# Optimization experiments

Hardware: AMD Instinct MI355X
Metric: run time of the kernel (lower is better)

The kernel has to match this reference:

```python
import jax, jax.numpy as jnp
import numpy as np

N_NODES = 50000
N_EDGES = 800000
IN_DIM = 128
E_FEATS = 64
H = 8
D = IN_DIM // H
NEG_SLOPE = 0.2


def setup_inputs() -> dict:
    key = jax.random.key(0)
    ks = jax.random.split(key, 9)
    h = jax.random.normal(ks[0], (N_NODES, IN_DIM), dtype=jnp.float32)
    edge_features = jax.random.normal(ks[1], (N_EDGES, E_FEATS), dtype=jnp.float32)
    src = jax.random.randint(ks[2], (N_EDGES,), 0, N_NODES, dtype=jnp.int32)
    dst = jax.random.randint(ks[3], (N_EDGES,), 0, N_NODES, dtype=jnp.int32)
    s = 0.05
    Wq = jax.random.normal(ks[4], (IN_DIM, IN_DIM), dtype=jnp.float32) * s
    Wk = jax.random.normal(ks[5], (IN_DIM, IN_DIM), dtype=jnp.float32) * s
    Wv = jax.random.normal(ks[6], (IN_DIM, IN_DIM), dtype=jnp.float32) * s
    We = jax.random.normal(ks[7], (H, E_FEATS), dtype=jnp.float32) * s
    Wres = jax.random.normal(ks[8], (IN_DIM, IN_DIM), dtype=jnp.float32) * s
    return {"h": h, "edge_features": edge_features, "src": src, "dst": dst,
            "Wq": Wq, "Wk": Wk, "Wv": Wv, "We": We, "Wres": Wres}


def reference(h, edge_features, src, dst, Wq, Wk, Wv, We, Wres):
    N = h.shape[0]
    # QKV projections (feat_drop is identity at eval)
    q = (h @ Wq.T).reshape(N, H, D)
    k = (h @ Wk.T).reshape(N, H, D)
    v = (h @ Wv.T).reshape(N, H, D)
    # ee / m_att are computed in the original forward but never used (dead code)
    _ee = edge_features @ We.T  # [E, H]

    # v_dot_u('q','k'): dot(q[dst], k[src]) per edge, per head -> [E, H]
    e = jnp.einsum('ehd,ehd->eh', q[dst], k[src])
    e = jnp.where(e >= 0, e, NEG_SLOPE * e)  # leaky_relu

    # edge_softmax over incoming edges of each destination node
    m = jax.ops.segment_max(e, dst, num_segments=N)          # [N, H]
    ex = jnp.exp(e - m[dst])                                 # [E, H]
    z = jax.ops.segment_sum(ex, dst, num_segments=N)         # [N, H]
    alpha = ex / z[dst]                                      # [E, H] (attn_drop identity)

    # weighted aggregation: sum_e alpha * v[src]
    msg = v[src] * alpha[:, :, None]                         # [E, H, D]
    rst = jax.ops.segment_sum(msg, dst, num_segments=N)      # [N, H, D]
    rst = rst.reshape(N, H * D)
    rst = rst + h @ Wres.T                                   # residual
    return rst
```

## Files before the change

kernel.cpp:

```cpp
#include <hip/hip_runtime.h>


#define NEG_SLOPE 0.2f
#define CB 1024

typedef __attribute__((ext_vector_type(8))) short short8;
typedef __attribute__((ext_vector_type(4))) float f32x4;

__device__ __forceinline__ unsigned short f2bf(float f) {
    unsigned int u = __builtin_bit_cast(unsigned int, f);
    u = (u + 0x7fffu + ((u >> 16) & 1u)) >> 16;
    return (unsigned short)u;
}
__device__ __forceinline__ float bf2f(unsigned short s) {
    unsigned int u = (unsigned int)s << 16;
    return __builtin_bit_cast(float, u);
}

__global__ __launch_bounds__(256) void zero_wconv_kernel(
    const float* __restrict__ Wq, const float* __restrict__ Wk,
    const float* __restrict__ Wv, const float* __restrict__ Wres,
    unsigned short* __restrict__ wpk, int* __restrict__ cnt,
    int* __restrict__ csr_pad, int n4)
{
    int t = blockIdx.x * 256 + threadIdx.x;
    if (t < 8192) {
        int l = t & 63;
        int v = t >> 6;
        int kk = v & 3;
        int wct = v >> 2;
        int ct = wct & 7;
        int w = wct >> 3;
        const float* W = (w == 0) ? Wq : (w == 1) ? Wk : (w == 2) ? Wv : Wres;
        const float* srcp = W + (size_t)(ct * 16 + (l & 15)) * 128 + kk * 32 + (l >> 4) * 8;
        float4 lo = *reinterpret_cast<const float4*>(srcp);
        float4 hi = *reinterpret_cast<const float4*>(srcp + 4);
        short8 o;
        o[0] = (short)f2bf(lo.x); o[1] = (short)f2bf(lo.y);
        o[2] = (short)f2bf(lo.z); o[3] = (short)f2bf(lo.w);
        o[4] = (short)f2bf(hi.x); o[5] = (short)f2bf(hi.y);
        o[6] = (short)f2bf(hi.z); o[7] = (short)f2bf(hi.w);
        *reinterpret_cast<short8*>(wpk + (size_t)t * 8) = o;
        if (t < 64) csr_pad[t] = 0;
    } else {
        int u = t - 8192;
        if (u < n4) reinterpret_cast<int4*>(cnt)[u] = make_int4(0, 0, 0, 0);
    }
}

__global__ __launch_bounds__(256) void proj_count_kernel(
    const float* __restrict__ h,
    const unsigned short* __restrict__ wpk,
    unsigned short* __restrict__ qb, unsigned short* __restrict__ kb,
    signed char* __restrict__ vi8, float* __restrict__ vscl,
    unsigned short* __restrict__ resb,
    const int* __restrict__ dst, int* __restrict__ cnt,
    int N, int E, int PB)
{
    if (blockIdx.x >= PB) {
        int start = (blockIdx.x - PB) * 256 + threadIdx.x;
        for (int e = start; e < E; e += CB * 256)
            atomicAdd(&cnt[dst[e]], 1);
        return;
    }

    const int wid = threadIdx.x >> 6;
    const int lane = threadIdx.x & 63;
    const int row0 = blockIdx.x * 128 + wid * 32;
    const int r = lane & 15, g = lane >> 4;

    short8 afrag[2][4];
    #pragma unroll
    for (int grp = 0; grp < 2; ++grp) {
        int arow = row0 + grp * 16 + r;
        if (arow >= N) arow = N - 1;
        const float* hrow = h + (size_t)arow * 128 + g * 8;
        #pragma unroll
        for (int kk = 0; kk < 4; ++kk) {
            float4 lo = *reinterpret_cast<const float4*>(hrow + kk * 32);
            float4 hi = *reinterpret_cast<const float4*>(hrow + kk * 32 + 4);
            short8 a;
            a[0] = (short)f2bf(lo.x); a[1] = (short)f2bf(lo.y);
            a[2] = (short)f2bf(lo.z); a[3] = (short)f2bf(lo.w);
            a[4] = (short)f2bf(hi.x); a[5] = (short)f2bf(hi.y);
            a[6] = (short)f2bf(hi.z); a[7] = (short)f2bf(hi.w);
            afrag[grp][kk] = a;
        }
    }

    #pragma unroll
    for (int sec = 0; sec < 3; ++sec) {
        const int w = (sec == 0) ? 0 : (sec == 1) ? 1 : 3;
        unsigned short* O = (sec == 0) ? qb : (sec == 1) ? kb : resb;
        #pragma unroll
        for (int ct = 0; ct < 8; ++ct) {
            const unsigned short* bp =
                wpk + ((size_t)((w * 8 + ct) * 4) * 64 + lane) * 8;
            f32x4 acc[2];
            acc[0] = (f32x4)(0.f); acc[1] = (f32x4)(0.f);
            #pragma unroll
            for (int kk = 0; kk < 4; ++kk) {
                short8 bfrag = *reinterpret_cast<const short8*>(bp + (size_t)kk * 512);
                acc[0] = __builtin_amdgcn_mfma_f32_16x16x32_bf16(
                    afrag[0][kk], bfrag, acc[0], 0, 0, 0);
                acc[1] = __builtin_amdgcn_mfma_f32_16x16x32_bf16(
                    afrag[1][kk], bfrag, acc[1], 0, 0, 0);
            }
            #pragma unroll
            for (int grp = 0; grp < 2; ++grp)
                #pragma unroll
                for (int j = 0; j < 4; ++j) {
                    int orow = row0 + grp * 16 + g * 4 + j;
                    if (orow < N)
                        O[(size_t)orow * 128 + ct * 16 + r] = f2bf(acc[grp][j]);
                }
        }
    }

    {
        f32x4 av[2][8];
        #pragma unroll
        for (int grp = 0; grp < 2; ++grp)
            #pragma unroll
            for (int ct = 0; ct < 8; ++ct) av[grp][ct] = (f32x4)(0.f);

        #pragma unroll
        for (int ct = 0; ct < 8; ++ct) {
            const unsigned short* bp =
                wpk + ((size_t)((2 * 8 + ct) * 4) * 64 + lane) * 8;
            #pragma unroll
            for (int kk = 0; kk < 4; ++kk) {
                short8 bfrag = *reinterpret_cast<const short8*>(bp + (size_t)kk * 512);
                av[0][ct] = __builtin_amdgcn_mfma_f32_16x16x32_bf16(
                    afrag[0][kk], bfrag, av[0][ct], 0, 0, 0);
                av[1][ct] = __builtin_amdgcn_mfma_f32_16x16x32_bf16(
                    afrag[1][kk], bfrag, av[1][ct], 0, 0, 0);
            }
        }

        #pragma unroll
        for (int grp = 0; grp < 2; ++grp)
            #pragma unroll
            for (int j = 0; j < 4; ++j) {
                int orow = row0 + grp * 16 + g * 4 + j;
                float m = fabsf(av[grp][0][j]);
                #pragma unroll
                for (int ct = 1; ct < 8; ++ct)
                    m = fmaxf(m, fabsf(av[grp][ct][j]));
                #pragma unroll
                for (int s = 1; s < 16; s <<= 1)
                    m = fmaxf(m, __shfl_xor(m, s, 64));
                float scale = m * (1.f / 127.f);
                float inv = (m > 0.f) ? 127.f / m : 0.f;
                if (orow < N) {
                    #pragma unroll
                    for (int ct = 0; ct < 8; ++ct) {
                        int qv = (int)rintf(av[grp][ct][j] * inv);
                        vi8[(size_t)orow * 128 + ct * 16 + r] = (signed char)qv;
                    }
                    if (r == 0) vscl[orow] = scale;
                }
            }
    }
}

__global__ __launch_bounds__(256) void blocksum_kernel(
    const int* __restrict__ cnt, int* __restrict__ bsum, int N)
{
    __shared__ int ws[4];
    const int tid = threadIdx.x;
    int base = blockIdx.x * 1024 + tid * 4;
    int s = 0;
    if (base + 3 < N) {
        int4 v = *reinterpret_cast<const int4*>(cnt + base);
        s = v.x + v.y + v.z + v.w;
    } else {
        for (int i = 0; i < 4; ++i)
            if (base + i < N) s += cnt[base + i];
    }
    #pragma unroll
    for (int m = 32; m >= 1; m >>= 1) s += __shfl_xor(s, m, 64);
    if ((tid & 63) == 0) ws[tid >> 6] = s;
    __syncthreads();
    if (tid == 0) bsum[blockIdx.x] = ws[0] + ws[1] + ws[2] + ws[3];
}

__global__ __launch_bounds__(256) void scanfinal_kernel(
    const int* __restrict__ cnt, const int* __restrict__ bsum,
    int* __restrict__ row_start, int* __restrict__ cursor,
    int N, int E, int NB)
{
    __shared__ int sboff;
    __shared__ int wsum[4];
    const int tid = threadIdx.x, lane = tid & 63, w = tid >> 6;

    if (tid < 64) {
        int v = (tid < NB && tid < blockIdx.x) ? bsum[tid] : 0;
        #pragma unroll
        for (int m = 32; m >= 1; m >>= 1) v += __shfl_xor(v, m, 64);
        if (tid == 0) sboff = v;
    }
    __syncthreads();

    int base = blockIdx.x * 1024 + tid * 4;
    int a0 = 0, a1 = 0, a2 = 0, a3 = 0;
    if (base + 3 < N) {
        int4 v = *reinterpret_cast<const int4*>(cnt + base);
        a0 = v.x; a1 = v.y; a2 = v.z; a3 = v.w;
    } else {
        if (base + 0 < N) a0 = cnt[base + 0];
        if (base + 1 < N) a1 = cnt[base + 1];
        if (base + 2 < N) a2 = cnt[base + 2];
        if (base + 3 < N) a3 = cnt[base + 3];
    }
    const int tsum = a0 + a1 + a2 + a3;
    int v = tsum;
    #pragma unroll
    for (int off = 1; off < 64; off <<= 1) {
        int t = __shfl_up(v, off, 64);
        if (lane >= off) v += t;
    }
    if (lane == 63) wsum[w] = v;
    __syncthreads();
    int woff = 0;
    for (int i = 0; i < w; ++i) woff += wsum[i];
    int run = sboff + woff + v - tsum;

    int r0 = run, r1 = run + a0, r2 = r1 + a1, r3 = r2 + a2;
    if (base + 3 < N) {
        int4 o = make_int4(r0, r1, r2, r3);
        *reinterpret_cast<int4*>(row_start + base) = o;
        *reinterpret_cast<int4*>(cursor + base) = o;
    } else {
        int rr[4] = {r0, r1, r2, r3};
        for (int i = 0; i < 4; ++i)
            if (base + i < N) { row_start[base + i] = rr[i]; cursor[base + i] = rr[i]; }
    }
    if (blockIdx.x == 0 && tid == 0) row_start[N] = E;
}

__global__ __launch_bounds__(256) void scatter_kernel(
    const int* __restrict__ src, const int* __restrict__ dst,
    int* __restrict__ cursor, int* __restrict__ csr_src, int E)
{
    int e = blockIdx.x * 256 + threadIdx.x;
    if (e < E) {
        int d = dst[e];
        int pos = atomicAdd(&cursor[d], 1);
        csr_src[pos] = src[e];
    }
}

__global__ __launch_bounds__(256) void fused_agg_kernel(
    const unsigned short* __restrict__ qb,
    const unsigned short* __restrict__ kb,
    const unsigned int* __restrict__ vi8_32,
    const float* __restrict__ vscl,
    const unsigned short* __restrict__ resb,
    const int* __restrict__ row_start, const int* __restrict__ csr_src,
    float* __restrict__ rst, int N)
{
    const int lane = threadIdx.x & 63;
    const int j = lane & 31;
    const int half = lane >> 5;
    const int node = blockIdx.x * 4 + (threadIdx.x >> 6);
    if (node >= N) return;

    const int beg = row_start[node];
    const int nE  = row_start[node + 1] - beg;
    const int* cp = csr_src + beg;

    ushort4 qraw = *reinterpret_cast<const ushort4*>(qb + (size_t)node * 128 + 4 * j);
    const float q0 = bf2f(qraw.x), q1 = bf2f(qraw.y),
                q2 = bf2f(qraw.z), q3 = bf2f(qraw.w);

    float zA = 0.f, zB = 0.f;
    float aA0 = 0.f, aA1 = 0.f, aA2 = 0.f, aA3 = 0.f;
    float aB0 = 0.f, aB1 = 0.f, aB2 = 0.f, aB3 = 0.f;

    if (nE > 0) {
        int sa = cp[half];
        int sb = cp[half + 2];

        for (int i = 0; i < nE; i += 4) {
            const int ii = i + half;
            const float m0 = (ii < nE) ? 1.f : 0.f;
            const float m1 = (ii + 2 < nE) ? 1.f : 0.f;
            const int s0 = sa, s1 = sb;
            sa = cp[ii + 4];
            sb = cp[ii + 6];

            ushort4 k0 = *reinterpret_cast<const ushort4*>(kb + (size_t)s0 * 128 + 4 * j);
            ushort4 k1 = *reinterpret_cast<const ushort4*>(kb + (size_t)s1 * 128 + 4 * j);
            unsigned int w0 = vi8_32[(size_t)s0 * 32 + j];
            unsigned int w1 = vi8_32[(size_t)s1 * 32 + j];
            float sv0 = vscl[s0];
            float sv1 = vscl[s1];

            float p0 = q0 * bf2f(k0.x) + q1 * bf2f(k0.y)
                     + q2 * bf2f(k0.z) + q3 * bf2f(k0.w);
            float p1 = q0 * bf2f(k1.x) + q1 * bf2f(k1.y)
                     + q2 * bf2f(k1.z) + q3 * bf2f(k1.w);
            p0 += __shfl_xor(p0, 1, 64);
            p0 += __shfl_xor(p0, 2, 64);
            p1 += __shfl_xor(p1, 1, 64);
            p1 += __shfl_xor(p1, 2, 64);
            float e0 = (p0 >= 0.f) ? p0 : NEG_SLOPE * p0;
            float e1 = (p1 >= 0.f) ? p1 : NEG_SLOPE * p1;
            e0 = m0 * __expf(e0);
            e1 = m1 * __expf(e1);
            zA += e0;
            zB += e1;
            const float f0 = e0 * sv0;
            const float f1 = e1 * sv1;
            aA0 = fmaf(f0, (float)(signed char)(w0),       aA0);
            aA1 = fmaf(f0, (float)(signed char)(w0 >> 8),  aA1);
            aA2 = fmaf(f0, (float)(signed char)(w0 >> 16), aA2);
            aA3 = fmaf(f0, (float)(signed char)(w0 >> 24), aA3);
            aB0 = fmaf(f1, (float)(signed char)(w1),       aB0);
            aB1 = fmaf(f1, (float)(signed char)(w1 >> 8),  aB1);
            aB2 = fmaf(f1, (float)(signed char)(w1 >> 16), aB2);
            aB3 = fmaf(f1, (float)(signed char)(w1 >> 24), aB3);
        }
    }

    float a0 = aA0 + aB0, a1 = aA1 + aB1, a2 = aA2 + aB2, a3 = aA3 + aB3;
    float z = zA + zB;
    a0 += __shfl_xor(a0, 32, 64);
    a1 += __shfl_xor(a1, 32, 64);
    a2 += __shfl_xor(a2, 32, 64);
    a3 += __shfl_xor(a3, 32, 64);
    z  += __shfl_xor(z, 32, 64);

    if (half == 0) {
        const size_t base = (size_t)node * 128 + 4 * j;
        ushort4 rb = *reinterpret_cast<const ushort4*>(resb + base);
        float inv = (nE > 0) ? 1.f / z : 0.f;
        float4 rv;
        rv.x = fmaf(a0, inv, bf2f(rb.x));
        rv.y = fmaf(a1, inv, bf2f(rb.y));
        rv.z = fmaf(a2, inv, bf2f(rb.z));
        rv.w = fmaf(a3, inv, bf2f(rb.w));
        *reinterpret_cast<float4*>(rst + base) = rv;
    }
}

extern "C" void kernel_launch(void* const* d_in, const int* in_sizes, int n_in,
                              void* d_out, int out_size, void* d_ws, size_t ws_size,
                              hipStream_t stream) {
    const float* h    = (const float*)d_in[0];
    const int*   src  = (const int*)d_in[2];
    const int*   dst  = (const int*)d_in[3];
    const float* Wq   = (const float*)d_in[4];
    const float* Wk   = (const float*)d_in[5];
    const float* Wv   = (const float*)d_in[6];
    const float* Wres = (const float*)d_in[8];
    float* rst = (float*)d_out;

    const int N = in_sizes[0] / 128;
    const int E = in_sizes[2];

    unsigned short* qb   = (unsigned short*)d_ws;
    unsigned short* kb   = qb + (size_t)N * 128;
    unsigned short* resb = kb + (size_t)N * 128;
    signed char*    vi8  = (signed char*)(resb + (size_t)N * 128);
    float*          vscl = (float*)(vi8 + (size_t)N * 128);
    unsigned short* wpk  = (unsigned short*)(vscl + N);
    int* cnt       = (int*)(wpk + 4 * 16384);
    int* row_start = cnt + N;
    int* cursor    = row_start + (N + 1);
    int* csr_src   = cursor + N;
    int* bsum      = csr_src + E + 64;

    const int n4 = N / 4;
    const int NB = (N + 1023) / 1024;
    const int PB = (N + 127) / 128;

    zero_wconv_kernel<<<(8192 + n4 + 255) / 256, 256, 0, stream>>>(
        Wq, Wk, Wv, Wres, wpk, cnt, csr_src + E, n4);
    proj_count_kernel<<<PB + CB, 256, 0, stream>>>(
        h, wpk, qb, kb, vi8, vscl, resb, dst, cnt, N, E, PB);
    blocksum_kernel<<<NB, 256, 0, stream>>>(cnt, bsum, N);
    scanfinal_kernel<<<NB, 256, 0, stream>>>(cnt, bsum, row_start, cursor,
                                             N, E, NB);
    scatter_kernel<<<(E + 255) / 256, 256, 0, stream>>>(src, dst, cursor,
                                                        csr_src, E);
    fused_agg_kernel<<<(N + 3) / 4, 256, 0, stream>>>(
        qb, kb, (const unsigned int*)vi8, vscl, resb, row_start, csr_src,
        rst, N);
}
```

Baseline: 166.6 us.

## Merge scan, scatter and aggregation into one cooperative persistent kernel

Replaces the blocksum, scanfinal, scatter and fused aggregation launches with a single cooperative kernel that runs a fixed grid of 1024 blocks and separates the phases with grid-wide syncs. The aim is to remove three kernel launch gaps and their tail effects. In exchange, the scatter and aggregation phases become grid-stride loops over a persistent grid, and each grid.sync adds its own barrier cost. Occupancy is now capped by the cooperative launch limits and the 4-blocks-per-CU launch bound.

```diff
diff --git a/kernel.cpp b/kernel.cpp
--- a/kernel.cpp
+++ b/kernel.cpp
@@ -1,8 +1,12 @@
 #include <hip/hip_runtime.h>
+#include <hip/hip_cooperative_groups.h>
+
+namespace cg = cooperative_groups;
 
 
 #define NEG_SLOPE 0.2f
 #define CB 1024
+#define GB 1024
 
 typedef __attribute__((ext_vector_type(8))) short short8;
 typedef __attribute__((ext_vector_type(4))) float f32x4;
@@ -164,184 +168,182 @@
     }
 }
 
-__global__ __launch_bounds__(256) void blocksum_kernel(
-    const int* __restrict__ cnt, int* __restrict__ bsum, int N)
-{
-    __shared__ int ws[4];
-    const int tid = threadIdx.x;
-    int base = blockIdx.x * 1024 + tid * 4;
-    int s = 0;
-    if (base + 3 < N) {
-        int4 v = *reinterpret_cast<const int4*>(cnt + base);
-        s = v.x + v.y + v.z + v.w;
-    } else {
-        for (int i = 0; i < 4; ++i)
-            if (base + i < N) s += cnt[base + i];
-    }
-    #pragma unroll
-    for (int m = 32; m >= 1; m >>= 1) s += __shfl_xor(s, m, 64);
-    if ((tid & 63) == 0) ws[tid >> 6] = s;
-    __syncthreads();
-    if (tid == 0) bsum[blockIdx.x] = ws[0] + ws[1] + ws[2] + ws[3];
-}
-
-__global__ __launch_bounds__(256) void scanfinal_kernel(
-    const int* __restrict__ cnt, const int* __restrict__ bsum,
-    int* __restrict__ row_start, int* __restrict__ cursor,
-    int N, int E, int NB)
-{
-    __shared__ int sboff;
-    __shared__ int wsum[4];
-    const int tid = threadIdx.x, lane = tid & 63, w = tid >> 6;
-
-    if (tid < 64) {
-        int v = (tid < NB && tid < blockIdx.x) ? bsum[tid] : 0;
-        #pragma unroll
-        for (int m = 32; m >= 1; m >>= 1) v += __shfl_xor(v, m, 64);
-        if (tid == 0) sboff = v;
-    }
-    __syncthreads();
-
-    int base = blockIdx.x * 1024 + tid * 4;
-    int a0 = 0, a1 = 0, a2 = 0, a3 = 0;
-    if (base + 3 < N) {
-        int4 v = *reinterpret_cast<const int4*>(cnt + base);
-        a0 = v.x; a1 = v.y; a2 = v.z; a3 = v.w;
-    } else {
-        if (base + 0 < N) a0 = cnt[base + 0];
-        if (base + 1 < N) a1 = cnt[base + 1];
-        if (base + 2 < N) a2 = cnt[base + 2];
-        if (base + 3 < N) a3 = cnt[base + 3];
-    }
-    const int tsum = a0 + a1 + a2 + a3;
-    int v = tsum;
-    #pragma unroll
-    for (int off = 1; off < 64; off <<= 1) {
-        int t = __shfl_up(v, off, 64);
-        if (lane >= off) v += t;
-    }
-    if (lane == 63) wsum[w] = v;
-    __syncthreads();
-    int woff = 0;
-    for (int i = 0; i < w; ++i) woff += wsum[i];
-    int run = sboff + woff + v - tsum;
-
-    int r0 = run, r1 = run + a0, r2 = r1 + a1, r3 = r2 + a2;
-    if (base + 3 < N) {
-        int4 o = make_int4(r0, r1, r2, r3);
-        *reinterpret_cast<int4*>(row_start + base) = o;
-        *reinterpret_cast<int4*>(cursor + base) = o;
-    } else {
-        int rr[4] = {r0, r1, r2, r3};
-        for (int i = 0; i < 4; ++i)
-            if (base + i < N) { row_start[base + i] = rr[i]; cursor[base + i] = rr[i]; }
-    }
-    if (blockIdx.x == 0 && tid == 0) row_start[N] = E;
-}
-
-__global__ __launch_bounds__(256) void scatter_kernel(
-    const int* __restrict__ src, const int* __restrict__ dst,
-    int* __restrict__ cursor, int* __restrict__ csr_src, int E)
-{
-    int e = blockIdx.x * 256 + threadIdx.x;
-    if (e < E) {
-        int d = dst[e];
-        int pos = atomicAdd(&cursor[d], 1);
-        csr_src[pos] = src[e];
-    }
-}
-
-__global__ __launch_bounds__(256) void fused_agg_kernel(
+__global__ __launch_bounds__(256, 4) void graph_coop_kernel(
     const unsigned short* __restrict__ qb,
     const unsigned short* __restrict__ kb,
     const unsigned int* __restrict__ vi8_32,
     const float* __restrict__ vscl,
     const unsigned short* __restrict__ resb,
-    const int* __restrict__ row_start, const int* __restrict__ csr_src,
-    float* __restrict__ rst, int N)
+    const int* __restrict__ src, const int* __restrict__ dst,
+    int* __restrict__ cnt, int* __restrict__ bsum,
+    int* __restrict__ row_start, int* __restrict__ cursor,
+    int* __restrict__ csr_src, float* __restrict__ rst,
+    int N, int E, int NB)
 {
-    const int lane = threadIdx.x & 63;
+    cg::grid_group grid = cg::this_grid();
+    const int tid = threadIdx.x;
+    const int lane = tid & 63;
+
+    if ((int)blockIdx.x < NB) {
+        __shared__ int ws[4];
+        int base = blockIdx.x * 1024 + tid * 4;
+        int s = 0;
+        if (base + 3 < N) {
+            int4 v = *reinterpret_cast<const int4*>(cnt + base);
+            s = v.x + v.y + v.z + v.w;
+        } else {
+            for (int i = 0; i < 4; ++i)
+                if (base + i < N) s += cnt[base + i];
+        }
+        #pragma unroll
+        for (int m = 32; m >= 1; m >>= 1) s += __shfl_xor(s, m, 64);
+        if ((tid & 63) == 0) ws[tid >> 6] = s;
+        __syncthreads();
+        if (tid == 0) bsum[blockIdx.x] = ws[0] + ws[1] + ws[2] + ws[3];
+    }
+    grid.sync();
+
+    if ((int)blockIdx.x < NB) {
+        __shared__ int sboff;
+        __shared__ int wsum[4];
+        const int w = tid >> 6;
+
+        if (tid < 64) {
+            int v = (tid < NB && tid < (int)blockIdx.x) ? bsum[tid] : 0;
+            #pragma unroll
+            for (int m = 32; m >= 1; m >>= 1) v += __shfl_xor(v, m, 64);
+            if (tid == 0) sboff = v;
+        }
+        __syncthreads();
+
+        int base = blockIdx.x * 1024 + tid * 4;
+        int a0 = 0, a1 = 0, a2 = 0, a3 = 0;
+        if (base + 3 < N) {
+            int4 v = *reinterpret_cast<const int4*>(cnt + base);
+            a0 = v.x; a1 = v.y; a2 = v.z; a3 = v.w;
+        } else {
+            if (base + 0 < N) a0 = cnt[base + 0];
+            if (base + 1 < N) a1 = cnt[base + 1];
+            if (base + 2 < N) a2 = cnt[base + 2];
+            if (base + 3 < N) a3 = cnt[base + 3];
+        }
+        const int tsum = a0 + a1 + a2 + a3;
+        int v = tsum;
+        #pragma unroll
+        for (int off = 1; off < 64; off <<= 1) {
+            int t2 = __shfl_up(v, off, 64);
+            if (lane >= off) v += t2;
+        }
+        if (lane == 63) wsum[w] = v;
+        __syncthreads();
+        int woff = 0;
+        for (int i = 0; i < w; ++i) woff += wsum[i];
+        int run = sboff + woff + v - tsum;
+
+        int r0 = run, r1 = run + a0, r2 = r1 + a1, r3 = r2 + a2;
+        if (base + 3 < N) {
+            int4 o = make_int4(r0, r1, r2, r3);
+            *reinterpret_cast<int4*>(row_start + base) = o;
+            *reinterpret_cast<int4*>(cursor + base) = o;
+        } else {
+            int rr[4] = {r0, r1, r2, r3};
+            for (int i = 0; i < 4; ++i)
+                if (base + i < N) { row_start[base + i] = rr[i]; cursor[base + i] = rr[i]; }
+        }
+        if (blockIdx.x == 0 && tid == 0) row_start[N] = E;
+    }
+    grid.sync();
+
+    for (int e = blockIdx.x * 256 + tid; e < E; e += GB * 256) {
+        int d = dst[e];
+        int pos = atomicAdd(&cursor[d], 1);
+        csr_src[pos] = src[e];
+    }
+    grid.sync();
+
     const int j = lane & 31;
     const int half = lane >> 5;
-    const int node = blockIdx.x * 4 + (threadIdx.x >> 6);
-    if (node >= N) return;
-
-    const int beg = row_start[node];
-    const int nE  = row_start[node + 1] - beg;
-    const int* cp = csr_src + beg;
-
-    ushort4 qraw = *reinterpret_cast<const ushort4*>(qb + (size_t)node * 128 + 4 * j);
-    const float q0 = bf2f(qraw.x), q1 = bf2f(qraw.y),
-                q2 = bf2f(qraw.z), q3 = bf2f(qraw.w);
-
-    float zA = 0.f, zB = 0.f;
-    float aA0 = 0.f, aA1 = 0.f, aA2 = 0.f, aA3 = 0.f;
-    float aB0 = 0.f, aB1 = 0.f, aB2 = 0.f, aB3 = 0.f;
-
-    if (nE > 0) {
-        int sa = cp[half];
-        int sb = cp[half + 2];
-
-        for (int i = 0; i < nE; i += 4) {
-            const int ii = i + half;
-            const float m0 = (ii < nE) ? 1.f : 0.f;
-            const float m1 = (ii + 2 < nE) ? 1.f : 0.f;
-            const int s0 = sa, s1 = sb;
-            sa = cp[ii + 4];
-            sb = cp[ii + 6];
-
-            ushort4 k0 = *reinterpret_cast<const ushort4*>(kb + (size_t)s0 * 128 + 4 * j);
-            ushort4 k1 = *reinterpret_cast<const ushort4*>(kb + (size_t)s1 * 128 + 4 * j);
-            unsigned int w0 = vi8_32[(size_t)s0 * 32 + j];
-            unsigned int w1 = vi8_32[(size_t)s1 * 32 + j];
-            float sv0 = vscl[s0];
-            float sv1 = vscl[s1];
-
-            float p0 = q0 * bf2f(k0.x) + q1 * bf2f(k0.y)
-                     + q2 * bf2f(k0.z) + q3 * bf2f(k0.w);
-            float p1 = q0 * bf2f(k1.x) + q1 * bf2f(k1.y)
-                     + q2 * bf2f(k1.z) + q3 * bf2f(k1.w);
-            p0 += __shfl_xor(p0, 1, 64);
-            p0 += __shfl_xor(p0, 2, 64);
-            p1 += __shfl_xor(p1, 1, 64);
-            p1 += __shfl_xor(p1, 2, 64);
-            float e0 = (p0 >= 0.f) ? p0 : NEG_SLOPE * p0;
-            float e1 = (p1 >= 0.f) ? p1 : NEG_SLOPE * p1;
-            e0 = m0 * __expf(e0);
-            e1 = m1 * __expf(e1);
-            zA += e0;
-            zB += e1;
-            const float f0 = e0 * sv0;
-            const float f1 = e1 * sv1;
-            aA0 = fmaf(f0, (float)(signed char)(w0),       aA0);
-            aA1 = fmaf(f0, (float)(signed char)(w0 >> 8),  aA1);
-            aA2 = fmaf(f0, (float)(signed char)(w0 >> 16), aA2);
-            aA3 = fmaf(f0, (float)(signed char)(w0 >> 24), aA3);
-            aB0 = fmaf(f1, (float)(signed char)(w1),       aB0);
-            aB1 = fmaf(f1, (float)(signed char)(w1 >> 8),  aB1);
-            aB2 = fmaf(f1, (float)(signed char)(w1 >> 16), aB2);
-            aB3 = fmaf(f1, (float)(signed char)(w1 >> 24), aB3);
-        }
-    }
-
-    float a0 = aA0 + aB0, a1 = aA1 + aB1, a2 = aA2 + aB2, a3 = aA3 + aB3;
-    float z = zA + zB;
-    a0 += __shfl_xor(a0, 32, 64);
-    a1 += __shfl_xor(a1, 32, 64);
-    a2 += __shfl_xor(a2, 32, 64);
-    a3 += __shfl_xor(a3, 32, 64);
-    z  += __shfl_xor(z, 32, 64);
-
-    if (half == 0) {
-        const size_t base = (size_t)node * 128 + 4 * j;
-        ushort4 rb = *reinterpret_cast<const ushort4*>(resb + base);
-        float inv = (nE > 0) ? 1.f / z : 0.f;
-        float4 rv;
-        rv.x = fmaf(a0, inv, bf2f(rb.x));
-        rv.y = fmaf(a1, inv, bf2f(rb.y));
-        rv.z = fmaf(a2, inv, bf2f(rb.z));
-        rv.w = fmaf(a3, inv, bf2f(rb.w));
-        *reinterpret_cast<float4*>(rst + base) = rv;
+    const int wid = tid >> 6;
+    const int nwaves = GB * 4;
+
+    for (int node = blockIdx.x * 4 + wid; node < N; node += nwaves) {
+        const int beg = row_start[node];
+        const int nE  = row_start[node + 1] - beg;
+        const int* cp = csr_src + beg;
+
+        ushort4 qraw = *reinterpret_cast<const ushort4*>(qb + (size_t)node * 128 + 4 * j);
+        const float q0 = bf2f(qraw.x), q1 = bf2f(qraw.y),
+                    q2 = bf2f(qraw.z), q3 = bf2f(qraw.w);
+
+        float zA = 0.f, zB = 0.f;
+        float aA0 = 0.f, aA1 = 0.f, aA2 = 0.f, aA3 = 0.f;
+        float aB0 = 0.f, aB1 = 0.f, aB2 = 0.f, aB3 = 0.f;
+
+        if (nE > 0) {
+            int sa = cp[half];
+            int sb = cp[half + 2];
+
+            for (int i = 0; i < nE; i += 4) {
+                const int ii = i + half;
+                const float m0 = (ii < nE) ? 1.f : 0.f;
+                const float m1 = (ii + 2 < nE) ? 1.f : 0.f;
+                const int s0 = sa, s1 = sb;
+                sa = cp[ii + 4];
+                sb = cp[ii + 6];
+
+                ushort4 k0 = *reinterpret_cast<const ushort4*>(kb + (size_t)s0 * 128 + 4 * j);
+                ushort4 k1 = *reinterpret_cast<const ushort4*>(kb + (size_t)s1 * 128 + 4 * j);
+                unsigned int w0 = vi8_32[(size_t)s0 * 32 + j];
+                unsigned int w1 = vi8_32[(size_t)s1 * 32 + j];
+                float sv0 = vscl[s0];
+                float sv1 = vscl[s1];
+
+                float p0 = q0 * bf2f(k0.x) + q1 * bf2f(k0.y)
+                         + q2 * bf2f(k0.z) + q3 * bf2f(k0.w);
+                float p1 = q0 * bf2f(k1.x) + q1 * bf2f(k1.y)
+                         + q2 * bf2f(k1.z) + q3 * bf2f(k1.w);
+                p0 += __shfl_xor(p0, 1, 64);
+                p0 += __shfl_xor(p0, 2, 64);
+                p1 += __shfl_xor(p1, 1, 64);
+                p1 += __shfl_xor(p1, 2, 64);
+                float e0 = (p0 >= 0.f) ? p0 : NEG_SLOPE * p0;
+                float e1 = (p1 >= 0.f) ? p1 : NEG_SLOPE * p1;
+                e0 = m0 * __expf(e0);
+                e1 = m1 * __expf(e1);
+                zA += e0;
+                zB += e1;
+                const float f0 = e0 * sv0;
+                const float f1 = e1 * sv1;
+                aA0 = fmaf(f0, (float)(signed char)(w0),       aA0);
+                aA1 = fmaf(f0, (float)(signed char)(w0 >> 8),  aA1);
+                aA2 = fmaf(f0, (float)(signed char)(w0 >> 16), aA2);
+                aA3 = fmaf(f0, (float)(signed char)(w0 >> 24), aA3);
+                aB0 = fmaf(f1, (float)(signed char)(w1),       aB0);
+                aB1 = fmaf(f1, (float)(signed char)(w1 >> 8),  aB1);
+                aB2 = fmaf(f1, (float)(signed char)(w1 >> 16), aB2);
+                aB3 = fmaf(f1, (float)(signed char)(w1 >> 24), aB3);
+            }
+        }
+
+        float a0 = aA0 + aB0, a1 = aA1 + aB1, a2 = aA2 + aB2, a3 = aA3 + aB3;
+        float z = zA + zB;
+        a0 += __shfl_xor(a0, 32, 64);
+        a1 += __shfl_xor(a1, 32, 64);
+        a2 += __shfl_xor(a2, 32, 64);
+        a3 += __shfl_xor(a3, 32, 64);
+        z  += __shfl_xor(z, 32, 64);
+
+        if (half == 0) {
+            const size_t base = (size_t)node * 128 + 4 * j;
+            ushort4 rb = *reinterpret_cast<const ushort4*>(resb + base);
+            float inv = (nE > 0) ? 1.f / z : 0.f;
+            float4 rv;
+            rv.x = fmaf(a0, inv, bf2f(rb.x));
+            rv.y = fmaf(a1, inv, bf2f(rb.y));
+            rv.z = fmaf(a2, inv, bf2f(rb.z));
+            rv.w = fmaf(a3, inv, bf2f(rb.w));
+            *reinterpret_cast<float4*>(rst + base) = rv;
+        }
     }
 }
 
@@ -357,8 +359,8 @@
     const float* Wres = (const float*)d_in[8];
     float* rst = (float*)d_out;
 
-    const int N = in_sizes[0] / 128;
-    const int E = in_sizes[2];
+    int N = in_sizes[0] / 128;
+    int E = in_sizes[2];
 
     unsigned short* qb   = (unsigned short*)d_ws;
     unsigned short* kb   = qb + (size_t)N * 128;
@@ -373,19 +375,21 @@
     int* bsum      = csr_src + E + 64;
 
     const int n4 = N / 4;
-    const int NB = (N + 1023) / 1024;
+    int NB = (N + 1023) / 1024;
     const int PB = (N + 127) / 128;
 
     zero_wconv_kernel<<<(8192 + n4 + 255) / 256, 256, 0, stream>>>(
         Wq, Wk, Wv, Wres, wpk, cnt, csr_src + E, n4);
     proj_count_kernel<<<PB + CB, 256, 0, stream>>>(
         h, wpk, qb, kb, vi8, vscl, resb, dst, cnt, N, E, PB);
-    blocksum_kernel<<<NB, 256, 0, stream>>>(cnt, bsum, N);
-    scanfinal_kernel<<<NB, 256, 0, stream>>>(cnt, bsum, row_start, cursor,
-                                             N, E, NB);
-    scatter_kernel<<<(E + 255) / 256, 256, 0, stream>>>(src, dst, cursor,
-                                                        csr_src, E);
-    fused_agg_kernel<<<(N + 3) / 4, 256, 0, stream>>>(
-        qb, kb, (const unsigned int*)vi8, vscl, resb, row_start, csr_src,
-        rst, N);
-}
+
+    const unsigned int* vi8_32 = (const unsigned int*)vi8;
+    void* args[] = {
+        (void*)&qb, (void*)&kb, (void*)&vi8_32, (void*)&vscl, (void*)&resb,
+        (void*)&src, (void*)&dst, (void*)&cnt, (void*)&bsum,
+        (void*)&row_start, (void*)&cursor, (void*)&csr_src, (void*)&rst,
+        (void*)&N, (void*)&E, (void*)&NB
+    };
+    hipLaunchCooperativeKernel((const void*)graph_coop_kernel,
+                               dim3(GB), dim3(256), args, 0, stream);
+}
```

Measured after the change: 536.2 us. +221.8%, slower.

## Quantize K to int8 and interleave with V into one gathered row

Applied to the files above, without the earlier changes.

K is now quantized to int8 with a per-row scale, like V already was, instead of being stored as bf16. K and V bytes are interleaved into a single 256-byte row per node, and their scales are packed as a float2. Each edge gather then fetches one 8-byte load plus one float2 instead of separate K, V and scale loads, which cuts random-access traffic in the aggregation kernel. The cost is reduced precision in the attention logits, which could push the output past the accuracy tolerance.

```diff
diff --git a/kernel.cpp b/kernel.cpp
--- a/kernel.cpp
+++ b/kernel.cpp
@@ -51,9 +51,8 @@
 __global__ __launch_bounds__(256) void proj_count_kernel(
     const float* __restrict__ h,
     const unsigned short* __restrict__ wpk,
-    unsigned short* __restrict__ qb, unsigned short* __restrict__ kb,
-    signed char* __restrict__ vi8, float* __restrict__ vscl,
-    unsigned short* __restrict__ resb,
+    unsigned short* __restrict__ qb, unsigned char* __restrict__ kvb,
+    float* __restrict__ kvscl, unsigned short* __restrict__ resb,
     const int* __restrict__ dst, int* __restrict__ cnt,
     int N, int E, int PB)
 {
@@ -89,9 +88,9 @@
     }
 
     #pragma unroll
-    for (int sec = 0; sec < 3; ++sec) {
-        const int w = (sec == 0) ? 0 : (sec == 1) ? 1 : 3;
-        unsigned short* O = (sec == 0) ? qb : (sec == 1) ? kb : resb;
+    for (int sec = 0; sec < 2; ++sec) {
+        const int w = (sec == 0) ? 0 : 3;
+        unsigned short* O = (sec == 0) ? qb : resb;
         #pragma unroll
         for (int ct = 0; ct < 8; ++ct) {
             const unsigned short* bp =
@@ -117,7 +116,9 @@
         }
     }
 
-    {
+    #pragma unroll
+    for (int sec = 0; sec < 2; ++sec) {
+        const int w = 1 + sec;
         f32x4 av[2][8];
         #pragma unroll
         for (int grp = 0; grp < 2; ++grp)
@@ -127,7 +128,7 @@
         #pragma unroll
         for (int ct = 0; ct < 8; ++ct) {
             const unsigned short* bp =
-                wpk + ((size_t)((2 * 8 + ct) * 4) * 64 + lane) * 8;
+                wpk + ((size_t)((w * 8 + ct) * 4) * 64 + lane) * 8;
             #pragma unroll
             for (int kk = 0; kk < 4; ++kk) {
                 short8 bfrag = *reinterpret_cast<const short8*>(bp + (size_t)kk * 512);
@@ -156,9 +157,10 @@
                     #pragma unroll
                     for (int ct = 0; ct < 8; ++ct) {
                         int qv = (int)rintf(av[grp][ct][j] * inv);
-                        vi8[(size_t)orow * 128 + ct * 16 + r] = (signed char)qv;
+                        kvb[(size_t)orow * 256 + 32 * ct + 8 * (r >> 2)
+                            + (r & 3) + sec * 4] = (unsigned char)(signed char)qv;
                     }
-                    if (r == 0) vscl[orow] = scale;
+                    if (r == 0) kvscl[2 * orow + sec] = scale;
                 }
             }
     }
@@ -253,9 +255,8 @@
 
 __global__ __launch_bounds__(256) void fused_agg_kernel(
     const unsigned short* __restrict__ qb,
-    const unsigned short* __restrict__ kb,
-    const unsigned int* __restrict__ vi8_32,
-    const float* __restrict__ vscl,
+    const unsigned char* __restrict__ kvb,
+    const float2* __restrict__ kvscl,
     const unsigned short* __restrict__ resb,
     const int* __restrict__ row_start, const int* __restrict__ csr_src,
     float* __restrict__ rst, int N)
@@ -290,37 +291,41 @@
             sa = cp[ii + 4];
             sb = cp[ii + 6];
 
-            ushort4 k0 = *reinterpret_cast<const ushort4*>(kb + (size_t)s0 * 128 + 4 * j);
-            ushort4 k1 = *reinterpret_cast<const ushort4*>(kb + (size_t)s1 * 128 + 4 * j);
-            unsigned int w0 = vi8_32[(size_t)s0 * 32 + j];
-            unsigned int w1 = vi8_32[(size_t)s1 * 32 + j];
-            float sv0 = vscl[s0];
-            float sv1 = vscl[s1];
-
-            float p0 = q0 * bf2f(k0.x) + q1 * bf2f(k0.y)
-                     + q2 * bf2f(k0.z) + q3 * bf2f(k0.w);
-            float p1 = q0 * bf2f(k1.x) + q1 * bf2f(k1.y)
-                     + q2 * bf2f(k1.z) + q3 * bf2f(k1.w);
+            uint2 kv0 = *reinterpret_cast<const uint2*>(kvb + (size_t)s0 * 256 + 8 * j);
+            uint2 kv1 = *reinterpret_cast<const uint2*>(kvb + (size_t)s1 * 256 + 8 * j);
+            float2 sc0 = kvscl[s0];
+            float2 sc1 = kvscl[s1];
+
+            float p0 = q0 * (float)(signed char)(kv0.x)
+                     + q1 * (float)(signed char)(kv0.x >> 8)
+                     + q2 * (float)(signed char)(kv0.x >> 16)
+                     + q3 * (float)(signed char)(kv0.x >> 24);
+            float p1 = q0 * (float)(signed char)(kv1.x)
+                     + q1 * (float)(signed char)(kv1.x >> 8)
+                     + q2 * (float)(signed char)(kv1.x >> 16)
+                     + q3 * (float)(signed char)(kv1.x >> 24);
             p0 += __shfl_xor(p0, 1, 64);
             p0 += __shfl_xor(p0, 2, 64);
             p1 += __shfl_xor(p1, 1, 64);
             p1 += __shfl_xor(p1, 2, 64);
+            p0 *= sc0.x;
+            p1 *= sc1.x;
             float e0 = (p0 >= 0.f) ? p0 : NEG_SLOPE * p0;
             float e1 = (p1 >= 0.f) ? p1 : NEG_SLOPE * p1;
             e0 = m0 * __expf(e0);
             e1 = m1 * __expf(e1);
             zA += e0;
             zB += e1;
-            const float f0 = e0 * sv0;
-            const float f1 = e1 * sv1;
-            aA0 = fmaf(f0, (float)(signed char)(w0),       aA0);
-            aA1 = fmaf(f0, (float)(signed char)(w0 >> 8),  aA1);
-            aA2 = fmaf(f0, (float)(signed char)(w0 >> 16), aA2);
-            aA3 = fmaf(f0, (float)(signed char)(w0 >> 24), aA3);
-            aB0 = fmaf(f1, (float)(signed char)(w1),       aB0);
-            aB1 = fmaf(f1, (float)(signed char)(w1 >> 8),  aB1);
-            aB2 = fmaf(f1, (float)(signed char)(w1 >> 16), aB2);
-            aB3 = fmaf(f1, (float)(signed char)(w1 >> 24), aB3);
+            const float f0 = e0 * sc0.y;
+            const float f1 = e1 * sc1.y;
+            aA0 = fmaf(f0, (float)(signed char)(kv0.y),       aA0);
+            aA1 = fmaf(f0, (float)(signed char)(kv0.y >> 8),  aA1);
+            aA2 = fmaf(f0, (float)(signed char)(kv0.y >> 16), aA2);
+            aA3 = fmaf(f0, (float)(signed char)(kv0.y >> 24), aA3);
+            aB0 = fmaf(f1, (float)(signed char)(kv1.y),       aB0);
+            aB1 = fmaf(f1, (float)(signed char)(kv1.y >> 8),  aB1);
+            aB2 = fmaf(f1, (float)(signed char)(kv1.y >> 16), aB2);
+            aB3 = fmaf(f1, (float)(signed char)(kv1.y >> 24), aB3);
         }
     }
 
@@ -361,11 +366,10 @@
     const int E = in_sizes[2];
 
     unsigned short* qb   = (unsigned short*)d_ws;
-    unsigned short* kb   = qb + (size_t)N * 128;
-    unsigned short* resb = kb + (size_t)N * 128;
-    signed char*    vi8  = (signed char*)(resb + (size_t)N * 128);
-    float*          vscl = (float*)(vi8 + (size_t)N * 128);
-    unsigned short* wpk  = (unsigned short*)(vscl + N);
+    unsigned short* resb = qb + (size_t)N * 128;
+    unsigned char*  kvb  = (unsigned char*)(resb + (size_t)N * 128);
+    float*          kvscl = (float*)(kvb + (size_t)N * 256);
+    unsigned short* wpk  = (unsigned short*)(kvscl + 2 * N);
     int* cnt       = (int*)(wpk + 4 * 16384);
     int* row_start = cnt + N;
     int* cursor    = row_start + (N + 1);
@@ -379,13 +383,12 @@
     zero_wconv_kernel<<<(8192 + n4 + 255) / 256, 256, 0, stream>>>(
         Wq, Wk, Wv, Wres, wpk, cnt, csr_src + E, n4);
     proj_count_kernel<<<PB + CB, 256, 0, stream>>>(
-        h, wpk, qb, kb, vi8, vscl, resb, dst, cnt, N, E, PB);
+        h, wpk, qb, kvb, kvscl, resb, dst, cnt, N, E, PB);
     blocksum_kernel<<<NB, 256, 0, stream>>>(cnt, bsum, N);
     scanfinal_kernel<<<NB, 256, 0, stream>>>(cnt, bsum, row_start, cursor,
                                              N, E, NB);
     scatter_kernel<<<(E + 255) / 256, 256, 0, stream>>>(src, dst, cursor,
                                                         csr_src, E);
     fused_agg_kernel<<<(N + 3) / 4, 256, 0, stream>>>(
-        qb, kb, (const unsigned int*)vi8, vscl, resb, row_start, csr_src,
-        rst, N);
-}
+        qb, kvb, (const float2*)kvscl, resb, row_start, csr_src, rst, N);
+}
```

Measured after the change: 159.0 us. 1.05x faster.
